# Performance work log

Measured on AMD Instinct MI355X. Metric: run time of the kernel, lower is better.

Reference implementation:

```python
import jax, jax.numpy as jnp
import numpy as np

N = 16384      # number of points (pixels)
C = 64         # value channels of U
D_REF = 5      # bilateral reference feature dim (xy + rgb)


def setup_inputs() -> dict:
    key = jax.random.key(0)
    k1, k2 = jax.random.split(key)
    U = jax.random.normal(k1, (N, C), dtype=jnp.float32)
    ref = jax.random.normal(k2, (N, D_REF), dtype=jnp.float32)
    return {"U": U, "ref": ref}


def reference(U, ref):
    # Gaussian filtering on reference features (exact form of the LSH-approx filter):
    #   out[i] = sum_j exp(-0.5 * ||ref_i - ref_j||^2) * U[j]  -  U[i]
    sq = jnp.sum(ref * ref, axis=-1)                      # [N]
    d2 = sq[:, None] + sq[None, :] - 2.0 * (ref @ ref.T)  # [N, N] squared distances
    K = jnp.exp(-0.5 * jnp.maximum(d2, 0.0))              # [N, N] Gaussian kernel
    return K @ U - U                                       # [N, C]
```

## Files before the change

kernel.cpp:

```cpp
#include <hip/hip_runtime.h>
#include <hip/hip_bf16.h>
#include <stdint.h>

#define N_PTS 16384
#define C_CH  64
#define D_REF 5
#define LOG2E 1.44269504088896340736f
#define IBLOCKS 128

typedef __attribute__((ext_vector_type(8))) short bf16x8;
typedef __attribute__((ext_vector_type(4))) float f32x4;

__device__ __forceinline__ unsigned short bf16rn(float v) {
    unsigned u = __builtin_bit_cast(unsigned, v) + 0x8000u;
    return (unsigned short)(u >> 16);
}
__device__ __forceinline__ float bf16tof(unsigned x) {
    return __builtin_bit_cast(float, x << 16);
}
__device__ __forceinline__ unsigned pack2bf16(float lo, float hi) {
    unsigned a = __builtin_bit_cast(unsigned, lo) + 0x8000u;
    unsigned b = __builtin_bit_cast(unsigned, hi) + 0x8000u;
    return __builtin_amdgcn_perm(b, a, 0x07060302u);
}
__device__ __forceinline__ unsigned cvt2(float lo, float hi) {
#if __has_builtin(__builtin_amdgcn_cvt_pk_bf16_f32)
    typedef __attribute__((ext_vector_type(2))) __bf16 bf162_t;
    bf162_t r = __builtin_amdgcn_cvt_pk_bf16_f32(lo, hi);
    return __builtin_bit_cast(unsigned, r);
#else
    return pack2bf16(lo, hi);
#endif
}
__device__ __forceinline__ float fast_exp2(float x) {
#if __has_builtin(__builtin_amdgcn_exp2f)
    return __builtin_amdgcn_exp2f(x);
#else
    return exp2f(x);
#endif
}
__device__ __forceinline__ void dma16(const unsigned short* g, unsigned short* l) {
#if __has_builtin(__builtin_amdgcn_global_load_lds)
    __builtin_amdgcn_global_load_lds(
        (const __attribute__((address_space(1))) unsigned int*)g,
        (__attribute__((address_space(3))) unsigned int*)l, 16, 0, 0);
#else
    const int lane = threadIdx.x & 63;
    *(uint4*)(l + lane * 8) = *(const uint4*)(g);
#endif
}

__global__ __launch_bounds__(256) void prep_all(
    const float* __restrict__ U, const float* __restrict__ ref,
    unsigned short* __restrict__ packA, unsigned short* __restrict__ packB,
    unsigned short* __restrict__ utPack)
{
    __shared__ unsigned short tile[64 * 80];
    const int bid = blockIdx.x;
    const int t   = threadIdx.x;

    if (bid < 512) {
        const int gid  = bid * 256 + t;
        const int half = gid >> 16;
        const int id   = gid & 0xFFFF;
        const int tile16 = id >> 6;
        const int lane = id & 63;
        const int q    = lane >> 4;
        const int m    = lane & 15;
        const int p = half ? (tile16 * 16 + m)
                           : ((tile16 >> 1) * 32 + (m >> 2) * 8 + (m & 3) + (tile16 & 1) * 4);

        const float* r = ref + (size_t)p * D_REF;
        float rv[5];
        float sq = 0.f;
#pragma unroll
        for (int d = 0; d < 5; ++d) { rv[d] = r[d]; sq += rv[d] * rv[d]; }
        const float h = -0.5f * LOG2E * sq;

        unsigned short bh[5], bl[5];
#pragma unroll
        for (int d = 0; d < 5; ++d) {
            const float base = half ? rv[d] * LOG2E : rv[d];
            bh[d] = bf16rn(base);
            bl[d] = bf16rn(base - bf16tof((unsigned)bh[d]));
        }
        const unsigned short hh  = bf16rn(h);
        const unsigned short hl  = bf16rn(h - bf16tof((unsigned)hh));
        const unsigned short one = 0x3F80;

        unsigned short outv[8];
#pragma unroll
        for (int tt = 0; tt < 8; ++tt) {
            const int k = q * 8 + tt;
            unsigned short v = 0;
            if (!half) {
                if      (k < 5)   v = bh[k];
                else if (k < 10)  v = bh[k - 5];
                else if (k < 15)  v = bl[k - 10];
                else if (k == 15) v = hh;
                else if (k == 16) v = hl;
                else if (k <= 18) v = one;
            } else {
                if      (k < 5)   v = bh[k];
                else if (k < 10)  v = bl[k - 5];
                else if (k < 15)  v = bh[k - 10];
                else if (k <= 16) v = one;
                else if (k == 17) v = hh;
                else if (k == 18) v = hl;
            }
            outv[tt] = v;
        }
        unsigned short* dst = (half ? packB : packA) + ((size_t)tile16 * 64 + lane) * 8;
        *(uint4*)dst = *(uint4*)outv;
    } else {
        const int b  = bid - 512;
        const int j0 = b * 64;
        const int c  = t & 63;
        const int jb = t >> 6;
#pragma unroll
        for (int k = 0; k < 16; ++k) {
            const int jr = jb + k * 4;
            tile[c * 80 + jr] = bf16rn(U[(size_t)(j0 + jr) * C_CH + c]);
        }
        __syncthreads();
#pragma unroll
        for (int rep = 0; rep < 2; ++rep) {
            const int id   = rep * 256 + t;
            const int lane = id & 63;
            const int ct   = (id >> 6) & 3;
            const int kt   = id >> 8;
            const int m    = lane & 15;
            const int q    = lane >> 4;
            const uint4 frag = *(const uint4*)&tile[(ct * 16 + m) * 80 + kt * 32 + q * 8];
            const int jtile  = b * 2 + kt;
            *(uint4*)&utPack[(((size_t)jtile * 4 + ct) * 64 + lane) * 8] = frag;
        }
    }
}

template<int JS>
__global__ __launch_bounds__(256, 6) void lsh_main(
    const float* __restrict__ U,
    const unsigned short* __restrict__ packA,
    const unsigned short* __restrict__ packB,
    const unsigned short* __restrict__ utPack,
    unsigned short* __restrict__ part,
    float* __restrict__ out,
    int use_part)
{
    constexpr int CHUNKS = (N_PTS / JS) / 128;
    __shared__ __align__(16) unsigned short sh[12288];

    const int t    = threadIdx.x;
    const int lane = t & 63;
    const int wave = t >> 6;
    const int q    = lane >> 4;
    const int m    = lane & 15;

    const int ib = blockIdx.x / JS;
    const int js = blockIdx.x % JS;

    bf16x8 bfrag[2];
#pragma unroll
    for (int s = 0; s < 2; ++s) {
        const int itile = ib * 8 + wave * 2 + s;
        bfrag[s] = *(const bf16x8*)(packB + ((size_t)itile * 64 + lane) * 8);
    }

    f32x4 acc[2][4];
#pragma unroll
    for (int s = 0; s < 2; ++s)
#pragma unroll
        for (int ct = 0; ct < 4; ++ct) acc[s][ct] = (f32x4){0.f, 0.f, 0.f, 0.f};

    for (int chunk = 0; chunk < CHUNKS; ++chunk) {
        const unsigned short* srcU = utPack + (size_t)(js * CHUNKS + chunk) * 8192;
        const unsigned short* srcA = packA  + (size_t)(js * CHUNKS + chunk) * 4096;
        __syncthreads();
#pragma unroll
        for (int r = 0; r < 4; ++r)
            dma16(srcU + r * 2048 + wave * 512 + lane * 8, sh + r * 2048 + wave * 512);
#pragma unroll
        for (int r = 0; r < 2; ++r)
            dma16(srcA + r * 2048 + wave * 512 + lane * 8, sh + 8192 + r * 2048 + wave * 512);
        __syncthreads();

#pragma unroll
        for (int kt = 0; kt < 4; ++kt) {
            const bf16x8 ga0 = *(const bf16x8*)(sh + 8192 + (kt * 2 + 0) * 512 + lane * 8);
            const bf16x8 ga1 = *(const bf16x8*)(sh + 8192 + (kt * 2 + 1) * 512 + lane * 8);
            bf16x8 uf[4];
#pragma unroll
            for (int ct = 0; ct < 4; ++ct)
                uf[ct] = *(const bf16x8*)(sh + kt * 2048 + ct * 512 + lane * 8);

            const f32x4 z = (f32x4){0.f, 0.f, 0.f, 0.f};
#pragma unroll
            for (int s = 0; s < 2; ++s) {
                const f32x4 g0 = __builtin_amdgcn_mfma_f32_16x16x32_bf16(ga0, bfrag[s], z, 0, 0, 0);
                const f32x4 g1 = __builtin_amdgcn_mfma_f32_16x16x32_bf16(ga1, bfrag[s], z, 0, 0, 0);
                union { unsigned u[4]; bf16x8 v; } sb;
                sb.u[0] = cvt2(fast_exp2(g0[0]), fast_exp2(g0[1]));
                sb.u[1] = cvt2(fast_exp2(g0[2]), fast_exp2(g0[3]));
                sb.u[2] = cvt2(fast_exp2(g1[0]), fast_exp2(g1[1]));
                sb.u[3] = cvt2(fast_exp2(g1[2]), fast_exp2(g1[3]));
#pragma unroll
                for (int ct = 0; ct < 4; ++ct)
                    acc[s][ct] = __builtin_amdgcn_mfma_f32_16x16x32_bf16(
                        uf[ct], sb.v, acc[s][ct], 0, 0, 0);
            }
        }
    }

    if (use_part) {
        unsigned short* dst = part + ((size_t)ib * JS + js) * 8192;
#pragma unroll
        for (int s = 0; s < 2; ++s)
#pragma unroll
            for (int cp = 0; cp < 2; ++cp) {
                uint4 w;
                w.x = cvt2(acc[s][cp*2+0][0], acc[s][cp*2+0][1]);
                w.y = cvt2(acc[s][cp*2+0][2], acc[s][cp*2+0][3]);
                w.z = cvt2(acc[s][cp*2+1][0], acc[s][cp*2+1][1]);
                w.w = cvt2(acc[s][cp*2+1][2], acc[s][cp*2+1][3]);
                *(uint4*)(dst + ((s * 2 + cp) * 256 + t) * 8) = w;
            }
    } else {
#pragma unroll
        for (int s = 0; s < 2; ++s) {
            const int i_glob = ib * 128 + (wave * 2 + s) * 16 + m;
#pragma unroll
            for (int ct = 0; ct < 4; ++ct)
#pragma unroll
                for (int r2 = 0; r2 < 4; ++r2) {
                    const int c = ct * 16 + q * 4 + r2;
                    float val = acc[s][ct][r2];
                    if (js == 0) val -= U[(size_t)i_glob * C_CH + c];
                    atomicAdd(&out[(size_t)i_glob * C_CH + c], val);
                }
        }
    }
}

template<int JS>
__global__ __launch_bounds__(256) void reduce_part(
    const unsigned short* __restrict__ part, const float* __restrict__ U,
    float* __restrict__ out)
{
    const int ib   = blockIdx.x >> 2;
    const int s2cp = blockIdx.x & 3;
    const int tt   = threadIdx.x;
    const int s  = s2cp >> 1, cp = s2cp & 1;
    const int wv = tt >> 6, ln = tt & 63, q = ln >> 4, m = ln & 15;
    const int i  = ib * 128 + (wv * 2 + s) * 16 + m;

    float sums[8];
#pragma unroll
    for (int e = 0; e < 8; ++e) sums[e] = 0.f;

    const unsigned short* base =
        part + (size_t)ib * JS * 8192 + (size_t)(s2cp * 256 + tt) * 8;
#pragma unroll
    for (int js = 0; js < JS; ++js) {
        const uint4 w = *(const uint4*)(base + (size_t)js * 8192);
        sums[0] += bf16tof(w.x & 0xFFFFu); sums[1] += bf16tof(w.x >> 16);
        sums[2] += bf16tof(w.y & 0xFFFFu); sums[3] += bf16tof(w.y >> 16);
        sums[4] += bf16tof(w.z & 0xFFFFu); sums[5] += bf16tof(w.z >> 16);
        sums[6] += bf16tof(w.w & 0xFFFFu); sums[7] += bf16tof(w.w >> 16);
    }

#pragma unroll
    for (int cti = 0; cti < 2; ++cti) {
        const int c0 = (cp * 2 + cti) * 16 + q * 4;
        const f32x4 u = *(const f32x4*)(U + (size_t)i * 64 + c0);
        f32x4 r;
        r[0] = sums[cti * 4 + 0] - u[0];
        r[1] = sums[cti * 4 + 1] - u[1];
        r[2] = sums[cti * 4 + 2] - u[2];
        r[3] = sums[cti * 4 + 3] - u[3];
        *(f32x4*)(out + (size_t)i * 64 + c0) = r;
    }
}

extern "C" void kernel_launch(void* const* d_in, const int* in_sizes, int n_in,
                              void* d_out, int out_size, void* d_ws, size_t ws_size,
                              hipStream_t stream) {
    const float* U   = (const float*)d_in[0];
    const float* ref = (const float*)d_in[1];
    float* out = (float*)d_out;

    unsigned short* utPack = (unsigned short*)d_ws;
    unsigned short* packA  = (unsigned short*)((char*)d_ws + (size_t)2 * 1024 * 1024);
    unsigned short* packB  = (unsigned short*)((char*)d_ws + (size_t)3 * 1024 * 1024);
    unsigned short* part   = (unsigned short*)((char*)d_ws + (size_t)4 * 1024 * 1024);

    const size_t MB = 1024 * 1024;
    prep_all<<<768, 256, 0, stream>>>(U, ref, packA, packB, utPack);

    if (ws_size >= 36 * MB) {
        lsh_main<16><<<IBLOCKS * 16, 256, 0, stream>>>(U, packA, packB, utPack,
                                                       part, out, 1);
        reduce_part<16><<<IBLOCKS * 4, 256, 0, stream>>>(part, U, out);
    } else {
        hipMemsetAsync(d_out, 0, (size_t)out_size * sizeof(float), stream);
        lsh_main<8><<<IBLOCKS * 8, 256, 0, stream>>>(U, packA, packB, utPack,
                                                     part, out, 0);
    }
}
```

Before: 122.0 us.

## Double-buffer LDS chunks and software-pipeline exp production with accumulation MFMAs

Halves the chunk size to 64 j-points and double-buffers LDS so the async DMA of the next chunk overlaps compute on the current one, replacing the two full barriers per chunk with explicit vmcnt waits. It also restructures the inner loop so the Gaussian-weight MFMA+exp for the next k-tile is interleaved with the accumulation MFMAs of the previous one. Launch bounds drop from 6 to 4 waves per SIMD to give registers for the extra in-flight fragments, trading occupancy for intra-wave overlap.

```diff
diff --git a/kernel.cpp b/kernel.cpp
--- a/kernel.cpp
+++ b/kernel.cpp
@@ -139,7 +139,7 @@
 }
 
 template<int JS>
-__global__ __launch_bounds__(256, 6) void lsh_main(
+__global__ __launch_bounds__(256, 4) void lsh_main(
     const float* __restrict__ U,
     const unsigned short* __restrict__ packA,
     const unsigned short* __restrict__ packB,
@@ -148,8 +148,8 @@
     float* __restrict__ out,
     int use_part)
 {
-    constexpr int CHUNKS = (N_PTS / JS) / 128;
-    __shared__ __align__(16) unsigned short sh[12288];
+    constexpr int CHUNKS = (N_PTS / JS) / 64;
+    __shared__ __align__(16) unsigned short sh[2][6144];
 
     const int t    = threadIdx.x;
     const int lane = t & 63;
@@ -173,43 +173,68 @@
 #pragma unroll
         for (int ct = 0; ct < 4; ++ct) acc[s][ct] = (f32x4){0.f, 0.f, 0.f, 0.f};
 
-    for (int chunk = 0; chunk < CHUNKS; ++chunk) {
-        const unsigned short* srcU = utPack + (size_t)(js * CHUNKS + chunk) * 8192;
-        const unsigned short* srcA = packA  + (size_t)(js * CHUNKS + chunk) * 4096;
-        __syncthreads();
-#pragma unroll
-        for (int r = 0; r < 4; ++r)
-            dma16(srcU + r * 2048 + wave * 512 + lane * 8, sh + r * 2048 + wave * 512);
-#pragma unroll
-        for (int r = 0; r < 2; ++r)
-            dma16(srcA + r * 2048 + wave * 512 + lane * 8, sh + 8192 + r * 2048 + wave * 512);
-        __syncthreads();
-
-#pragma unroll
-        for (int kt = 0; kt < 4; ++kt) {
-            const bf16x8 ga0 = *(const bf16x8*)(sh + 8192 + (kt * 2 + 0) * 512 + lane * 8);
-            const bf16x8 ga1 = *(const bf16x8*)(sh + 8192 + (kt * 2 + 1) * 512 + lane * 8);
-            bf16x8 uf[4];
-#pragma unroll
-            for (int ct = 0; ct < 4; ++ct)
-                uf[ct] = *(const bf16x8*)(sh + kt * 2048 + ct * 512 + lane * 8);
-
-            const f32x4 z = (f32x4){0.f, 0.f, 0.f, 0.f};
-#pragma unroll
-            for (int s = 0; s < 2; ++s) {
-                const f32x4 g0 = __builtin_amdgcn_mfma_f32_16x16x32_bf16(ga0, bfrag[s], z, 0, 0, 0);
-                const f32x4 g1 = __builtin_amdgcn_mfma_f32_16x16x32_bf16(ga1, bfrag[s], z, 0, 0, 0);
-                union { unsigned u[4]; bf16x8 v; } sb;
-                sb.u[0] = cvt2(fast_exp2(g0[0]), fast_exp2(g0[1]));
-                sb.u[1] = cvt2(fast_exp2(g0[2]), fast_exp2(g0[3]));
-                sb.u[2] = cvt2(fast_exp2(g1[0]), fast_exp2(g1[1]));
-                sb.u[3] = cvt2(fast_exp2(g1[2]), fast_exp2(g1[3]));
-#pragma unroll
-                for (int ct = 0; ct < 4; ++ct)
-                    acc[s][ct] = __builtin_amdgcn_mfma_f32_16x16x32_bf16(
-                        uf[ct], sb.v, acc[s][ct], 0, 0, 0);
-            }
-        }
+    auto STAGE = [&](int chunk, int b) {
+        const unsigned short* srcU = utPack + (size_t)(js * CHUNKS + chunk) * 4096;
+        const unsigned short* srcA = packA  + (size_t)(js * CHUNKS + chunk) * 2048;
+        unsigned short* d = &sh[b][0];
+        dma16(srcU + wave * 512 + lane * 8,        d + wave * 512);
+        dma16(srcU + 2048 + wave * 512 + lane * 8, d + 2048 + wave * 512);
+        dma16(srcA + wave * 512 + lane * 8,        d + 4096 + wave * 512);
+    };
+    auto PROD = [&](const unsigned short* buf, int kt, bf16x8* sf) {
+        const bf16x8 ga0 = *(const bf16x8*)(buf + 4096 + kt * 1024 + lane * 8);
+        const bf16x8 ga1 = *(const bf16x8*)(buf + 4096 + kt * 1024 + 512 + lane * 8);
+        const f32x4 z = (f32x4){0.f, 0.f, 0.f, 0.f};
+#pragma unroll
+        for (int s = 0; s < 2; ++s) {
+            const f32x4 g0 = __builtin_amdgcn_mfma_f32_16x16x32_bf16(ga0, bfrag[s], z, 0, 0, 0);
+            const f32x4 g1 = __builtin_amdgcn_mfma_f32_16x16x32_bf16(ga1, bfrag[s], z, 0, 0, 0);
+            union { unsigned u[4]; bf16x8 v; } sb;
+            sb.u[0] = cvt2(fast_exp2(g0[0]), fast_exp2(g0[1]));
+            sb.u[1] = cvt2(fast_exp2(g0[2]), fast_exp2(g0[3]));
+            sb.u[2] = cvt2(fast_exp2(g1[0]), fast_exp2(g1[1]));
+            sb.u[3] = cvt2(fast_exp2(g1[2]), fast_exp2(g1[3]));
+            sf[s] = sb.v;
+        }
+    };
+    auto CONS = [&](const unsigned short* buf, int kt, const bf16x8* sf) {
+#pragma unroll
+        for (int ct = 0; ct < 4; ++ct) {
+            const bf16x8 uf = *(const bf16x8*)(buf + kt * 2048 + ct * 512 + lane * 8);
+#pragma unroll
+            for (int s = 0; s < 2; ++s)
+                acc[s][ct] = __builtin_amdgcn_mfma_f32_16x16x32_bf16(
+                    uf, sf[s], acc[s][ct], 0, 0, 0);
+        }
+    };
+
+    bf16x8 pA[2], pB[2];
+
+    STAGE(0, 0);
+    STAGE(1, 1);
+    asm volatile("s_waitcnt vmcnt(3)" ::: "memory");
+    __builtin_amdgcn_s_barrier();
+    PROD(&sh[0][0], 0, pA);
+
+    int cur = 0;
+    for (int c = 0; c < CHUNKS - 1; ++c) {
+        const unsigned short* bufc = &sh[cur][0];
+        const unsigned short* bufn = &sh[cur ^ 1][0];
+        PROD(bufc, 1, pB);
+        CONS(bufc, 0, pA);
+        asm volatile("s_waitcnt vmcnt(0)" ::: "memory");
+        __builtin_amdgcn_s_barrier();
+        PROD(bufn, 0, pA);
+        CONS(bufc, 1, pB);
+        __builtin_amdgcn_s_barrier();
+        if (c + 2 < CHUNKS) STAGE(c + 2, cur);
+        cur ^= 1;
+    }
+    {
+        const unsigned short* bufc = &sh[cur][0];
+        PROD(bufc, 1, pB);
+        CONS(bufc, 0, pA);
+        CONS(bufc, 1, pB);
     }
 
     if (use_part) {
```

Result: faster. 118.7 us (-2.7%).
